# Kernel tuning notes

Hardware: AMD Instinct MI355X
Metric: run time of the kernel (lower is better)

## Reference

```python
import jax, jax.numpy as jnp
import numpy as np

NUM_HEADS = 12
HIDDEN = 768
HEAD = HIDDEN // NUM_HEADS
SCALE = HIDDEN ** (-0.5)  # NB: module scales by hidden_dim**-0.5, not head_size**-0.5


def setup_inputs() -> dict:
    key = jax.random.key(0)
    ks = jax.random.split(key, 8)
    B, N = 16, 512
    std = HIDDEN ** (-0.5)
    return {
        "x": jax.random.normal(ks[0], (B, N, HIDDEN), dtype=jnp.float32),
        "encoding_bias": jax.random.normal(ks[1], (B, N, N), dtype=jnp.float32),
        "Wq": jax.random.normal(ks[2], (HIDDEN, HIDDEN), dtype=jnp.float32) * std,
        "Wk": jax.random.normal(ks[3], (HIDDEN, HIDDEN), dtype=jnp.float32) * std,
        "Wv": jax.random.normal(ks[4], (HIDDEN, HIDDEN), dtype=jnp.float32) * std,
        "bv": jax.random.normal(ks[5], (HIDDEN,), dtype=jnp.float32) * 0.01,
        "Wo": jax.random.normal(ks[6], (HIDDEN, HIDDEN), dtype=jnp.float32) * std,
        "bo": jax.random.normal(ks[7], (HIDDEN,), dtype=jnp.float32) * 0.01,
    }


def reference(x, encoding_bias, Wq, Wk, Wv, bv, Wo, bo):
    B, N, _ = x.shape
    # torch nn.Linear: y = x @ W.T (+ b)
    q = (x @ Wq.T).reshape(B, N, NUM_HEADS, HEAD)
    k = (x @ Wk.T).reshape(B, N, NUM_HEADS, HEAD)
    v = (x @ Wv.T + bv).reshape(B, N, NUM_HEADS, HEAD)
    # scores: [B, H, N, N] with additive graph bias broadcast over heads
    a = jnp.einsum("bnhd,bmhd->bhnm", q, k) * SCALE + encoding_bias[:, None, :, :]
    # data-dependent pad mask: rows whose scores are identically zero
    pad_mask = jnp.all(a == 0, axis=-1)  # [B, H, N]
    a = jnp.where(pad_mask[..., None], -jnp.inf, a)
    a = jax.nn.softmax(a, axis=-1)
    a = jnp.nan_to_num(a)  # all -inf rows -> NaN -> 0
    o = jnp.einsum("bhnm,bmhd->bnhd", a, v).reshape(B, N, HIDDEN)
    # dropout is identity in eval mode
    return o @ Wo.T + bo
```

## Files before the change

### kernel.cpp

```cpp
#include <hip/hip_runtime.h>
#include <stdint.h>

typedef unsigned short u16;
typedef unsigned int u32;
typedef __bf16 bf16x8 __attribute__((ext_vector_type(8)));
typedef float f32x4 __attribute__((ext_vector_type(4)));

#define NH 12
#define HD 64
#define SEQ 512
#define BATCH 16
#define HID 768
#define SCALE_Q 0.03608439182435161f

__device__ __forceinline__ u16 f2bf(float f) {
    u32 u = __builtin_bit_cast(u32, f);
    u32 r = (u + 0x7FFFu + ((u >> 16) & 1u)) >> 16;
    return (u16)r;
}

__device__ __forceinline__ void gl2lds16(const u16* g, u16* lds_base) {
    __builtin_amdgcn_global_load_lds(
        (const __attribute__((address_space(1))) u32*)g,
        (__attribute__((address_space(3))) u32*)lds_base, 16, 0, 0);
}

__global__ void cvt_kernel(const float* __restrict__ src, u16* __restrict__ dst) {
    int i = (blockIdx.x * 256 + threadIdx.x) * 4;
    float4 v = *(const float4*)(src + i);
    ushort4 o;
    o.x = f2bf(v.x); o.y = f2bf(v.y); o.z = f2bf(v.z); o.w = f2bf(v.w);
    *(ushort4*)(dst + i) = o;
}

__global__ void cvt4_kernel(const float* __restrict__ s0, const float* __restrict__ s1,
                            const float* __restrict__ s2, const float* __restrict__ s3,
                            u16* __restrict__ d0, u16* __restrict__ d1,
                            u16* __restrict__ d2, u16* __restrict__ d3) {
    int y = blockIdx.y;
    const float* s = (y == 0) ? s0 : (y == 1) ? s1 : (y == 2) ? s2 : s3;
    u16* d = (y == 0) ? d0 : (y == 1) ? d1 : (y == 2) ? d2 : d3;
    int i = (blockIdx.x * 256 + threadIdx.x) * 4;
    float4 v = *(const float4*)(s + i);
    ushort4 o;
    o.x = f2bf(v.x); o.y = f2bf(v.y); o.z = f2bf(v.z); o.w = f2bf(v.w);
    *(ushort4*)(d + i) = o;
}

__device__ __forceinline__ void gemm_mainloop(
    const u16* __restrict__ Ag, const u16* __restrict__ Bg,
    u16* As, u16* Bs, f32x4 (&acc)[4][4])
{
    const int tid = threadIdx.x;
    const int l = tid & 63, w = tid >> 6;
    const int wm = w & 1, wn = w >> 1;
    const int lr = l & 15, lg = l >> 4;

    const int c0 = tid, c1 = tid + 256;
    const int r0 = c0 >> 2, q0 = (c0 & 3) * 8;
    const int r1 = c1 >> 2, q1 = (c1 & 3) * 8;
    u16* Alds0 = As + w * 512;
    u16* Alds1 = As + 2048 + w * 512;
    u16* Blds0 = Bs + w * 512;
    u16* Blds1 = Bs + 2048 + w * 512;

    for (int k0 = 0; k0 < HID; k0 += 32) {
        __syncthreads();
        gl2lds16(Ag + (size_t)r0 * HID + k0 + q0, Alds0);
        gl2lds16(Ag + (size_t)r1 * HID + k0 + q1, Alds1);
        gl2lds16(Bg + (size_t)r0 * HID + k0 + q0, Blds0);
        gl2lds16(Bg + (size_t)r1 * HID + k0 + q1, Blds1);
        __syncthreads();

        bf16x8 af[4], bfr[4];
#pragma unroll
        for (int mi = 0; mi < 4; mi++)
            af[mi] = *(const bf16x8*)(As + (wm * 64 + mi * 16 + lr) * 32 + lg * 8);
#pragma unroll
        for (int ni = 0; ni < 4; ni++)
            bfr[ni] = *(const bf16x8*)(Bs + (wn * 64 + ni * 16 + lr) * 32 + lg * 8);
#pragma unroll
        for (int mi = 0; mi < 4; mi++)
#pragma unroll
            for (int ni = 0; ni < 4; ni++)
                acc[mi][ni] = __builtin_amdgcn_mfma_f32_16x16x32_bf16(af[mi], bfr[ni], acc[mi][ni], 0, 0, 0);
    }
}

__global__ __launch_bounds__(256, 2) void gemm_qkv(
    const u16* __restrict__ xb, const u16* __restrict__ wq,
    const u16* __restrict__ wk, const u16* __restrict__ wv,
    const float* __restrict__ bv,
    u16* __restrict__ qb, u16* __restrict__ kb, u16* __restrict__ vtb)
{
    __shared__ __align__(16) u16 As[128 * 32];
    __shared__ __align__(16) u16 Bs[128 * 32];
    const int tid = threadIdx.x;
    const int l = tid & 63, w = tid >> 6;
    const int wm = w & 1, wn = w >> 1;
    const int lr = l & 15, lg = l >> 4;
    const int mt = blockIdx.x, nt = blockIdx.y, z = blockIdx.z;

    const u16* Bw = (z == 0) ? wq : (z == 1) ? wk : wv;
    const u16* Ag = xb + (size_t)(mt * 128) * HID;
    const u16* Bg = Bw + (size_t)(nt * 128) * HID;

    f32x4 acc[4][4] = {};
    gemm_mainloop(Ag, Bg, As, Bs, acc);

#pragma unroll
    for (int mi = 0; mi < 4; mi++) {
#pragma unroll
        for (int ni = 0; ni < 4; ni++) {
            const int jg = nt * 128 + wn * 64 + ni * 16 + lr;
            const int h = jg >> 6, d = jg & 63;
            if (z < 2) {
                u16* O = (z == 0) ? qb : kb;
#pragma unroll
                for (int r = 0; r < 4; r++) {
                    int ig = mt * 128 + wm * 64 + mi * 16 + lg * 4 + r;
                    int b = ig >> 9, n = ig & 511;
                    O[((size_t)(b * NH + h) * SEQ + n) * HD + d] = f2bf(acc[mi][ni][r]);
                }
            } else {
                float bb = bv[jg];
                int i0 = mt * 128 + wm * 64 + mi * 16 + lg * 4;
                int b = i0 >> 9, m = i0 & 511;
                ushort4 pk;
                pk.x = f2bf(acc[mi][ni][0] + bb);
                pk.y = f2bf(acc[mi][ni][1] + bb);
                pk.z = f2bf(acc[mi][ni][2] + bb);
                pk.w = f2bf(acc[mi][ni][3] + bb);
                *(ushort4*)(vtb + ((size_t)(b * NH + h) * HD + d) * SEQ + m) = pk;
            }
        }
    }
}

__global__ __launch_bounds__(256, 2) void gemm_out(
    const u16* __restrict__ A, const u16* __restrict__ wo,
    const float* __restrict__ bo, float* __restrict__ Cout)
{
    __shared__ __align__(16) u16 As[128 * 32];
    __shared__ __align__(16) u16 Bs[128 * 32];
    const int tid = threadIdx.x;
    const int l = tid & 63, w = tid >> 6;
    const int wm = w & 1, wn = w >> 1;
    const int lr = l & 15, lg = l >> 4;
    const int mt = blockIdx.x, nt = blockIdx.y;

    const u16* Ag = A + (size_t)(mt * 128) * HID;
    const u16* Bg = wo + (size_t)(nt * 128) * HID;

    f32x4 acc[4][4] = {};
    gemm_mainloop(Ag, Bg, As, Bs, acc);

#pragma unroll
    for (int mi = 0; mi < 4; mi++) {
#pragma unroll
        for (int ni = 0; ni < 4; ni++) {
            const int jg = nt * 128 + wn * 64 + ni * 16 + lr;
            float bb = bo[jg];
#pragma unroll
            for (int r = 0; r < 4; r++) {
                int ig = mt * 128 + wm * 64 + mi * 16 + lg * 4 + r;
                Cout[(size_t)ig * HID + jg] = acc[mi][ni][r] + bb;
            }
        }
    }
}

#define LDA 88

__global__ __launch_bounds__(256, 2) void attn_kernel(
    const u16* __restrict__ qb, const u16* __restrict__ kb, const u16* __restrict__ vtb,
    const float* __restrict__ eb, u16* __restrict__ ob)
{
    __shared__ __align__(16) u16 Ks[64 * LDA];
    __shared__ __align__(16) u16 Vs[64 * LDA];
    __shared__ __align__(16) u16 Ps[4][16 * LDA];

    const int tid = threadIdx.x;
    const int l = tid & 63, w = tid >> 6;
    const int lr = l & 15, lg = l >> 4;
    const int qt = blockIdx.x, h = blockIdx.y, b = blockIdx.z;
    const int bh = b * NH + h;
    const int qrow0 = qt * 64 + w * 16;

    const u16* qptr = qb + ((size_t)bh * SEQ + qrow0 + lr) * HD;
    bf16x8 qf0 = *(const bf16x8*)(qptr + lg * 8);
    bf16x8 qf1 = *(const bf16x8*)(qptr + 32 + lg * 8);

    const u16* Kg = kb + (size_t)bh * SEQ * HD;
    const u16* Vg = vtb + (size_t)bh * HD * SEQ;
    const float* Eg = eb + ((size_t)b * SEQ + qrow0 + lg * 4) * SEQ;

    f32x4 oacc[4] = {};
    float run_m[4] = {-1e30f, -1e30f, -1e30f, -1e30f};
    float run_l[4] = {0.f, 0.f, 0.f, 0.f};
    int nzf[4] = {0, 0, 0, 0};

    const int c0 = tid, c1 = tid + 256;

    for (int mt0 = 0; mt0 < SEQ; mt0 += 64) {
        uint4 kv0 = *(const uint4*)(Kg + (size_t)(mt0 + (c0 >> 3)) * HD + (c0 & 7) * 8);
        uint4 kv1 = *(const uint4*)(Kg + (size_t)(mt0 + (c1 >> 3)) * HD + (c1 & 7) * 8);
        uint4 vv0 = *(const uint4*)(Vg + (size_t)(c0 >> 3) * SEQ + mt0 + (c0 & 7) * 8);
        uint4 vv1 = *(const uint4*)(Vg + (size_t)(c1 >> 3) * SEQ + mt0 + (c1 & 7) * 8);
        __syncthreads();
        *(uint4*)(Ks + (c0 >> 3) * LDA + (c0 & 7) * 8) = kv0;
        *(uint4*)(Ks + (c1 >> 3) * LDA + (c1 & 7) * 8) = kv1;
        *(uint4*)(Vs + (c0 >> 3) * LDA + (c0 & 7) * 8) = vv0;
        *(uint4*)(Vs + (c1 >> 3) * LDA + (c1 & 7) * 8) = vv1;
        __syncthreads();

        float sm[4][4];
#pragma unroll
        for (int mi = 0; mi < 4; mi++) {
            bf16x8 kf0 = *(const bf16x8*)(Ks + (mi * 16 + lr) * LDA + lg * 8);
            bf16x8 kf1 = *(const bf16x8*)(Ks + (mi * 16 + lr) * LDA + 32 + lg * 8);
            f32x4 s = {};
            s = __builtin_amdgcn_mfma_f32_16x16x32_bf16(qf0, kf0, s, 0, 0, 0);
            s = __builtin_amdgcn_mfma_f32_16x16x32_bf16(qf1, kf1, s, 0, 0, 0);
#pragma unroll
            for (int r = 0; r < 4; r++) {
                float sv = s[r] * SCALE_Q + Eg[(size_t)r * SEQ + mt0 + mi * 16 + lr];
                nzf[r] |= (sv != 0.0f);
                sm[mi][r] = sv;
            }
        }

        u16* Pw = Ps[w];
#pragma unroll
        for (int r = 0; r < 4; r++) {
            float tm = fmaxf(fmaxf(sm[0][r], sm[1][r]), fmaxf(sm[2][r], sm[3][r]));
            tm = fmaxf(tm, __shfl_xor(tm, 1));
            tm = fmaxf(tm, __shfl_xor(tm, 2));
            tm = fmaxf(tm, __shfl_xor(tm, 4));
            tm = fmaxf(tm, __shfl_xor(tm, 8));
            float nm = fmaxf(run_m[r], tm);
            float alpha = __expf(run_m[r] - nm);
            run_m[r] = nm;
            float ps = 0.f;
#pragma unroll
            for (int mi = 0; mi < 4; mi++) {
                float p = __expf(sm[mi][r] - nm);
                sm[mi][r] = p;
                ps += p;
            }
            ps += __shfl_xor(ps, 1);
            ps += __shfl_xor(ps, 2);
            ps += __shfl_xor(ps, 4);
            ps += __shfl_xor(ps, 8);
            run_l[r] = run_l[r] * alpha + ps;
#pragma unroll
            for (int di = 0; di < 4; di++) oacc[di][r] *= alpha;
        }
#pragma unroll
        for (int mi = 0; mi < 4; mi++)
#pragma unroll
            for (int r = 0; r < 4; r++)
                Pw[(lg * 4 + r) * LDA + mi * 16 + lr] = f2bf(sm[mi][r]);

#pragma unroll
        for (int ks = 0; ks < 2; ks++) {
            bf16x8 pf = *(const bf16x8*)(Pw + lr * LDA + ks * 32 + lg * 8);
#pragma unroll
            for (int di = 0; di < 4; di++) {
                bf16x8 vf = *(const bf16x8*)(Vs + (di * 16 + lr) * LDA + ks * 32 + lg * 8);
                oacc[di] = __builtin_amdgcn_mfma_f32_16x16x32_bf16(pf, vf, oacc[di], 0, 0, 0);
            }
        }
    }

#pragma unroll
    for (int r = 0; r < 4; r++) {
        int nz = nzf[r];
        nz |= __shfl_xor(nz, 1);
        nz |= __shfl_xor(nz, 2);
        nz |= __shfl_xor(nz, 4);
        nz |= __shfl_xor(nz, 8);
        float inv = nz ? (1.0f / run_l[r]) : 0.0f;
        int n = qrow0 + lg * 4 + r;
        u16* orow = ob + ((size_t)b * SEQ + n) * HID + h * HD;
#pragma unroll
        for (int di = 0; di < 4; di++)
            orow[di * 16 + lr] = f2bf(oacc[di][r] * inv);
    }
}

extern "C" void kernel_launch(void* const* d_in, const int* in_sizes, int n_in,
                              void* d_out, int out_size, void* d_ws, size_t ws_size,
                              hipStream_t stream) {
    (void)in_sizes; (void)n_in; (void)out_size; (void)ws_size;
    const float* x  = (const float*)d_in[0];
    const float* eb = (const float*)d_in[1];
    const float* Wq = (const float*)d_in[2];
    const float* Wk = (const float*)d_in[3];
    const float* Wv = (const float*)d_in[4];
    const float* bv = (const float*)d_in[5];
    const float* Wo = (const float*)d_in[6];
    const float* bo = (const float*)d_in[7];
    float* out = (float*)d_out;

    const int NX = BATCH * SEQ * HID;
    const int NW = HID * HID;
    u16* ws   = (u16*)d_ws;
    u16* xb   = ws;
    u16* wqb  = xb + NX;
    u16* wkb  = wqb + NW;
    u16* wvb  = wkb + NW;
    u16* wob  = wvb + NW;
    u16* qb   = wob + NW;
    u16* kb   = qb + NX;
    u16* vtb  = kb + NX;
    u16* obuf = vtb + NX;

    cvt_kernel<<<NX / 1024, 256, 0, stream>>>(x, xb);
    cvt4_kernel<<<dim3(NW / 1024, 4), 256, 0, stream>>>(Wq, Wk, Wv, Wo, wqb, wkb, wvb, wob);

    gemm_qkv<<<dim3(64, 6, 3), 256, 0, stream>>>(xb, wqb, wkb, wvb, bv, qb, kb, vtb);

    attn_kernel<<<dim3(8, NH, BATCH), 256, 0, stream>>>(qb, kb, vtb, eb, obuf);

    gemm_out<<<dim3(64, 6), 256, 0, stream>>>(obuf, wob, bo, out);
}
```

Before: 230.4 us.

## Pre-convert bias to bf16, fold scale into Q, async swizzled K/V LDS loads

Adds a pass that converts the encoding bias to bf16 so each of the 12 head blocks reads half the bytes, and loads the bias into the MFMA accumulator as its initial value. The softmax scale is folded into the Q projection epilogue. K/V tiles now go straight from global memory to LDS with an XOR-swizzled unpadded layout, and the launch bounds are raised for more occupancy. Risks: the extra conversion pass over the 16.8 MB bias, bf16 rounding of the bias and of the scaled Q, and register spills from the higher occupancy targets.

After: 220.3 us. 1.05x faster.

```diff
diff --git a/kernel.cpp b/kernel.cpp
--- a/kernel.cpp
+++ b/kernel.cpp
@@ -17,6 +17,9 @@
     u32 u = __builtin_bit_cast(u32, f);
     u32 r = (u + 0x7FFFu + ((u >> 16) & 1u)) >> 16;
     return (u16)r;
+}
+__device__ __forceinline__ float bf2f(u16 h) {
+    return __builtin_bit_cast(float, (u32)h << 16);
 }
 
 __device__ __forceinline__ void gl2lds16(const u16* g, u16* lds_base) {
@@ -87,7 +90,7 @@
     }
 }
 
-__global__ __launch_bounds__(256, 2) void gemm_qkv(
+__global__ __launch_bounds__(256, 3) void gemm_qkv(
     const u16* __restrict__ xb, const u16* __restrict__ wq,
     const u16* __restrict__ wk, const u16* __restrict__ wv,
     const float* __restrict__ bv,
@@ -108,6 +111,7 @@
     f32x4 acc[4][4] = {};
     gemm_mainloop(Ag, Bg, As, Bs, acc);
 
+    const float sc = (z == 0) ? SCALE_Q : 1.0f;
 #pragma unroll
     for (int mi = 0; mi < 4; mi++) {
 #pragma unroll
@@ -120,7 +124,7 @@
                 for (int r = 0; r < 4; r++) {
                     int ig = mt * 128 + wm * 64 + mi * 16 + lg * 4 + r;
                     int b = ig >> 9, n = ig & 511;
-                    O[((size_t)(b * NH + h) * SEQ + n) * HD + d] = f2bf(acc[mi][ni][r]);
+                    O[((size_t)(b * NH + h) * SEQ + n) * HD + d] = f2bf(acc[mi][ni][r] * sc);
                 }
             } else {
                 float bb = bv[jg];
@@ -137,7 +141,7 @@
     }
 }
 
-__global__ __launch_bounds__(256, 2) void gemm_out(
+__global__ __launch_bounds__(256, 3) void gemm_out(
     const u16* __restrict__ A, const u16* __restrict__ wo,
     const float* __restrict__ bo, float* __restrict__ Cout)
 {
@@ -172,12 +176,12 @@
 
 #define LDA 88
 
-__global__ __launch_bounds__(256, 2) void attn_kernel(
+__global__ __launch_bounds__(256, 4) void attn_kernel(
     const u16* __restrict__ qb, const u16* __restrict__ kb, const u16* __restrict__ vtb,
-    const float* __restrict__ eb, u16* __restrict__ ob)
+    const u16* __restrict__ ebb, u16* __restrict__ ob)
 {
-    __shared__ __align__(16) u16 Ks[64 * LDA];
-    __shared__ __align__(16) u16 Vs[64 * LDA];
+    __shared__ __align__(16) u16 Ks[64 * 64];
+    __shared__ __align__(16) u16 Vs[64 * 64];
     __shared__ __align__(16) u16 Ps[4][16 * LDA];
 
     const int tid = threadIdx.x;
@@ -193,38 +197,50 @@
 
     const u16* Kg = kb + (size_t)bh * SEQ * HD;
     const u16* Vg = vtb + (size_t)bh * HD * SEQ;
-    const float* Eg = eb + ((size_t)b * SEQ + qrow0 + lg * 4) * SEQ;
+    const u16* Eg = ebb + ((size_t)b * SEQ + qrow0 + lg * 4) * SEQ;
 
     f32x4 oacc[4] = {};
     float run_m[4] = {-1e30f, -1e30f, -1e30f, -1e30f};
     float run_l[4] = {0.f, 0.f, 0.f, 0.f};
     int nzf[4] = {0, 0, 0, 0};
 
-    const int c0 = tid, c1 = tid + 256;
+    const int p0 = tid, p1 = tid + 256;
+    const int kr0 = p0 >> 3, kc0 = (p0 & 7) ^ (kr0 & 7);
+    const int kr1 = p1 >> 3, kc1 = (p1 & 7) ^ (kr1 & 7);
+    u16* Ks0 = Ks + w * 512;
+    u16* Ks1 = Ks + 2048 + w * 512;
+    u16* Vs0 = Vs + w * 512;
+    u16* Vs1 = Vs + 2048 + w * 512;
 
     for (int mt0 = 0; mt0 < SEQ; mt0 += 64) {
-        uint4 kv0 = *(const uint4*)(Kg + (size_t)(mt0 + (c0 >> 3)) * HD + (c0 & 7) * 8);
-        uint4 kv1 = *(const uint4*)(Kg + (size_t)(mt0 + (c1 >> 3)) * HD + (c1 & 7) * 8);
-        uint4 vv0 = *(const uint4*)(Vg + (size_t)(c0 >> 3) * SEQ + mt0 + (c0 & 7) * 8);
-        uint4 vv1 = *(const uint4*)(Vg + (size_t)(c1 >> 3) * SEQ + mt0 + (c1 & 7) * 8);
+        u16 bl[4][4];
+#pragma unroll
+        for (int mi = 0; mi < 4; mi++)
+#pragma unroll
+            for (int r = 0; r < 4; r++)
+                bl[mi][r] = Eg[(size_t)r * SEQ + mt0 + mi * 16 + lr];
+
         __syncthreads();
-        *(uint4*)(Ks + (c0 >> 3) * LDA + (c0 & 7) * 8) = kv0;
-        *(uint4*)(Ks + (c1 >> 3) * LDA + (c1 & 7) * 8) = kv1;
-        *(uint4*)(Vs + (c0 >> 3) * LDA + (c0 & 7) * 8) = vv0;
-        *(uint4*)(Vs + (c1 >> 3) * LDA + (c1 & 7) * 8) = vv1;
+        gl2lds16(Kg + (size_t)(mt0 + kr0) * HD + kc0 * 8, Ks0);
+        gl2lds16(Kg + (size_t)(mt0 + kr1) * HD + kc1 * 8, Ks1);
+        gl2lds16(Vg + (size_t)kr0 * SEQ + mt0 + kc0 * 8, Vs0);
+        gl2lds16(Vg + (size_t)kr1 * SEQ + mt0 + kc1 * 8, Vs1);
         __syncthreads();
 
         float sm[4][4];
 #pragma unroll
         for (int mi = 0; mi < 4; mi++) {
-            bf16x8 kf0 = *(const bf16x8*)(Ks + (mi * 16 + lr) * LDA + lg * 8);
-            bf16x8 kf1 = *(const bf16x8*)(Ks + (mi * 16 + lr) * LDA + 32 + lg * 8);
-            f32x4 s = {};
+            const int row = mi * 16 + lr;
+            bf16x8 kf0 = *(const bf16x8*)(Ks + row * 64 + ((lg ^ (row & 7)) * 8));
+            bf16x8 kf1 = *(const bf16x8*)(Ks + row * 64 + (((4 + lg) ^ (row & 7)) * 8));
+            f32x4 s;
+#pragma unroll
+            for (int r = 0; r < 4; r++) s[r] = bf2f(bl[mi][r]);
             s = __builtin_amdgcn_mfma_f32_16x16x32_bf16(qf0, kf0, s, 0, 0, 0);
             s = __builtin_amdgcn_mfma_f32_16x16x32_bf16(qf1, kf1, s, 0, 0, 0);
 #pragma unroll
             for (int r = 0; r < 4; r++) {
-                float sv = s[r] * SCALE_Q + Eg[(size_t)r * SEQ + mt0 + mi * 16 + lr];
+                float sv = s[r];
                 nzf[r] |= (sv != 0.0f);
                 sm[mi][r] = sv;
             }
@@ -267,7 +283,8 @@
             bf16x8 pf = *(const bf16x8*)(Pw + lr * LDA + ks * 32 + lg * 8);
 #pragma unroll
             for (int di = 0; di < 4; di++) {
-                bf16x8 vf = *(const bf16x8*)(Vs + (di * 16 + lr) * LDA + ks * 32 + lg * 8);
+                const int row = di * 16 + lr;
+                bf16x8 vf = *(const bf16x8*)(Vs + row * 64 + (((ks * 4 + lg) ^ (row & 7)) * 8));
                 oacc[di] = __builtin_amdgcn_mfma_f32_16x16x32_bf16(pf, vf, oacc[di], 0, 0, 0);
             }
         }
@@ -305,6 +322,7 @@
 
     const int NX = BATCH * SEQ * HID;
     const int NW = HID * HID;
+    const int NE = BATCH * SEQ * SEQ;
     u16* ws   = (u16*)d_ws;
     u16* xb   = ws;
     u16* wqb  = xb + NX;
@@ -315,13 +333,15 @@
     u16* kb   = qb + NX;
     u16* vtb  = kb + NX;
     u16* obuf = vtb + NX;
+    u16* ebb  = obuf + NX;
 
     cvt_kernel<<<NX / 1024, 256, 0, stream>>>(x, xb);
+    cvt_kernel<<<NE / 1024, 256, 0, stream>>>(eb, ebb);
     cvt4_kernel<<<dim3(NW / 1024, 4), 256, 0, stream>>>(Wq, Wk, Wv, Wo, wqb, wkb, wvb, wob);
 
     gemm_qkv<<<dim3(64, 6, 3), 256, 0, stream>>>(xb, wqb, wkb, wvb, bv, qb, kb, vtb);
 
-    attn_kernel<<<dim3(8, NH, BATCH), 256, 0, stream>>>(qb, kb, vtb, eb, obuf);
+    attn_kernel<<<dim3(8, NH, BATCH), 256, 0, stream>>>(qb, kb, vtb, ebb, obuf);
 
     gemm_out<<<dim3(64, 6), 256, 0, stream>>>(obuf, wob, bo, out);
 }
```
